# Kernel tuning notes

Measured on AMD Instinct MI355X. Metric: run time of the kernel, lower is better.

Reference implementation:

```python
import jax, jax.numpy as jnp
import numpy as np

EMB = 1024
HEADS = 16
DEPTH = EMB // HEADS
B, S = 8, 1024


def setup_inputs() -> dict:
    key = jax.random.key(0)
    ks = jax.random.split(key, 12)
    sc = 0.02
    return {
        "q": jax.random.normal(ks[0], (B, S, EMB), jnp.float32),
        "k": jax.random.normal(ks[1], (B, S, EMB), jnp.float32),
        "v": jax.random.normal(ks[2], (B, S, EMB), jnp.float32),
        # per-head Dense weights stacked: [H, EMB, DEPTH], biases [H, DEPTH]
        "Wq": jax.random.normal(ks[3], (HEADS, EMB, DEPTH), jnp.float32) * sc,
        "bq": jnp.zeros((HEADS, DEPTH), jnp.float32),
        "Wk": jax.random.normal(ks[4], (HEADS, EMB, DEPTH), jnp.float32) * sc,
        "bk": jnp.zeros((HEADS, DEPTH), jnp.float32),
        "Wv": jax.random.normal(ks[5], (HEADS, EMB, DEPTH), jnp.float32) * sc,
        "bv": jnp.zeros((HEADS, DEPTH), jnp.float32),
        # output Dense: [EMB, EMB], bias [EMB]
        "Wo": jax.random.normal(ks[6], (EMB, EMB), jnp.float32) * sc,
        "bo": jnp.zeros((EMB,), jnp.float32),
    }


def reference(q, k, v, Wq, bq, Wk, bk, Wv, bv, Wo, bo):
    # Per-head Dense projections, batched over heads via einsum.
    # qh: [B, H, S, DEPTH]
    qh = jnp.einsum("bsd,hde->bhse", q, Wq) + bq[None, :, None, :]
    kh = jnp.einsum("bsd,hde->bhse", k, Wk) + bk[None, :, None, :]
    vh = jnp.einsum("bsd,hde->bhse", v, Wv) + bv[None, :, None, :]
    # Scaled dot-product attention per head: logits [B, H, Sq, Sk]
    scale = 1.0 / jnp.sqrt(jnp.asarray(DEPTH, jnp.float32))
    logits = jnp.einsum("bhqe,bhke->bhqk", qh, kh) * scale
    attn = jax.nn.softmax(logits, axis=-1)
    ctx = jnp.einsum("bhqk,bhke->bhqe", attn, vh)  # [B, H, S, DEPTH]
    # concat heads along last axis (head order preserved)
    ctx = jnp.transpose(ctx, (0, 2, 1, 3)).reshape(B, S, EMB)
    return ctx @ Wo + bo
```

## Files before the change

### kernel.cpp

```cpp
#include <hip/hip_runtime.h>
#include <hip/hip_bf16.h>
#include <stdint.h>

typedef __bf16 bf16;
typedef __attribute__((ext_vector_type(8))) __bf16 bf16x8;
typedef __attribute__((ext_vector_type(4))) __bf16 bf16x4;
typedef __attribute__((ext_vector_type(4))) float f32x4;

#define GLD(g, l) __builtin_amdgcn_global_load_lds( \
    (const __attribute__((address_space(1))) void*)(g), \
    (__attribute__((address_space(3))) void*)(l), 16, 0, 0)

__device__ __forceinline__ f32x4 mfma16(bf16x8 a, bf16x8 b, f32x4 c) {
  return __builtin_amdgcn_mfma_f32_16x16x32_bf16(a, b, c, 0, 0, 0);
}
__device__ __forceinline__ float fexp2(float x) {
  return __builtin_amdgcn_exp2f(x);
}

__global__ void wtrans3(const float* __restrict__ Wq, const float* __restrict__ Wk,
                        const float* __restrict__ Wv, bf16* __restrict__ WT)
{
  __shared__ bf16 t[32][33];
  const int w = blockIdx.z;
  const float* W = (w == 0) ? Wq : (w == 1) ? Wk : Wv;
  const int h = blockIdx.x >> 1;
  const int c0 = (blockIdx.x & 1) * 32;
  const int r0 = blockIdx.y * 32;
  const float* s = W + (size_t)h * 65536;
  bf16* d = WT + (size_t)w * (1 << 20) + (size_t)h * 65536;
  const int tx = threadIdx.x, ty = threadIdx.y;
#pragma unroll
  for (int i = 0; i < 32; i += 8)
    t[ty + i][tx] = (bf16)s[(r0 + ty + i) * 64 + c0 + tx];
  __syncthreads();
#pragma unroll
  for (int i = 0; i < 32; i += 8)
    d[(c0 + ty + i) * 1024 + r0 + tx] = t[tx][ty + i];
}

__global__ void wtransO(const float* __restrict__ src, bf16* __restrict__ dst)
{
  __shared__ bf16 t[32][33];
  const int c0 = blockIdx.x * 32, r0 = blockIdx.y * 32;
  const int tx = threadIdx.x, ty = threadIdx.y;
#pragma unroll
  for (int i = 0; i < 32; i += 8)
    t[ty + i][tx] = (bf16)src[(r0 + ty + i) * 1024 + c0 + tx];
  __syncthreads();
#pragma unroll
  for (int i = 0; i < 32; i += 8)
    dst[(c0 + ty + i) * 1024 + r0 + tx] = t[tx][ty + i];
}

__global__ __launch_bounds__(256) void cast2(const float* __restrict__ q,
                                             const float* __restrict__ k,
                                             bf16* __restrict__ qc,
                                             bf16* __restrict__ kc)
{
  const float* s = blockIdx.y ? k : q;
  bf16* d = blockIdx.y ? kc : qc;
  const size_t i = ((size_t)blockIdx.x * 256 + threadIdx.x) * 8;
  float4 a = *(const float4*)(s + i);
  float4 b = *(const float4*)(s + i + 4);
  bf16x8 p;
  p[0] = (bf16)a.x; p[1] = (bf16)a.y; p[2] = (bf16)a.z; p[3] = (bf16)a.w;
  p[4] = (bf16)b.x; p[5] = (bf16)b.y; p[6] = (bf16)b.z; p[7] = (bf16)b.w;
  *(bf16x8*)(d + i) = p;
}

__global__ __launch_bounds__(256) void proj_qkv(
    const bf16* __restrict__ qc, const bf16* __restrict__ kc,
    const float* __restrict__ v, const bf16* __restrict__ WT,
    const float* __restrict__ bq, const float* __restrict__ bk,
    const float* __restrict__ bv, bf16* __restrict__ qh,
    bf16* __restrict__ kh, bf16* __restrict__ vt, float cscale)
{
  __shared__ bf16 S[16384];
  const int tid = threadIdx.x;
  const int wave = tid >> 6, lane = tid & 63;
  const int lr = lane & 15, quad = lane >> 4, kq = quad * 8;
  const int n0 = blockIdx.y * 128;
  const int mseg = blockIdx.x * 128;
  const int seg = mseg >> 13;
  const int m0 = mseg & 8191;
  const int wr = (wave >> 1) * 64, wc = (wave & 1) * 64;

  const float* bias = (seg == 0) ? bq : (seg == 1) ? bk : bv;
  const bf16* Bt = WT + (size_t)seg * (1 << 20);

  f32x4 acc[4][4];
#pragma unroll
  for (int i = 0; i < 4; i++)
#pragma unroll
    for (int j = 0; j < 4; j++)
#pragma unroll
      for (int e = 0; e < 4; e++) acc[i][j][e] = 0.f;

  const int srow = tid >> 2;
  const int sko = (tid & 3) * 8;
  const bf16* bPtr = Bt + (size_t)(n0 + srow) * 1024 + sko;

  if (seg < 2) {
    const bf16* Ab = (seg == 1) ? kc : qc;
    const bf16* aPtr = Ab + (size_t)(m0 + srow) * 1024 + sko;
    GLD(aPtr,             S + tid * 8);
    GLD(aPtr + 64 * 1024, S + 2048 + tid * 8);
    GLD(bPtr,             S + 4096 + tid * 8);
    GLD(bPtr + 64 * 1024, S + 6144 + tid * 8);
    for (int it = 0; it < 32; ++it) {
      const int p = it & 1;
      bf16* buf = S + p * 8192;
      bf16* nbuf = S + (p ^ 1) * 8192;
      __syncthreads();
      if (it + 1 < 32) {
        const int k0 = (it + 1) * 32;
        GLD(aPtr + k0,             nbuf + tid * 8);
        GLD(aPtr + 64 * 1024 + k0, nbuf + 2048 + tid * 8);
        GLD(bPtr + k0,             nbuf + 4096 + tid * 8);
        GLD(bPtr + 64 * 1024 + k0, nbuf + 6144 + tid * 8);
      }
      bf16x8 af[4], bfr[4];
#pragma unroll
      for (int i = 0; i < 4; i++) {
        af[i]  = *(const bf16x8*)(buf + (wr + i * 16 + lr) * 32 + kq);
        bfr[i] = *(const bf16x8*)(buf + 4096 + (wc + i * 16 + lr) * 32 + kq);
      }
#pragma unroll
      for (int im = 0; im < 4; im++)
#pragma unroll
        for (int in = 0; in < 4; in++)
          acc[im][in] = mfma16(af[im], bfr[in], acc[im][in]);
    }
  } else {
    const int ar = tid >> 1, ac2 = (tid & 1) * 16;
    const float* vPtr = v + (size_t)(m0 + ar) * 1024 + ac2;
    float4 f[4];
#pragma unroll
    for (int j = 0; j < 4; j++) f[j] = *(const float4*)(vPtr + j * 4);
    {
      bf16x8 p0, p1;
      p0[0]=(bf16)f[0].x; p0[1]=(bf16)f[0].y; p0[2]=(bf16)f[0].z; p0[3]=(bf16)f[0].w;
      p0[4]=(bf16)f[1].x; p0[5]=(bf16)f[1].y; p0[6]=(bf16)f[1].z; p0[7]=(bf16)f[1].w;
      p1[0]=(bf16)f[2].x; p1[1]=(bf16)f[2].y; p1[2]=(bf16)f[2].z; p1[3]=(bf16)f[2].w;
      p1[4]=(bf16)f[3].x; p1[5]=(bf16)f[3].y; p1[6]=(bf16)f[3].z; p1[7]=(bf16)f[3].w;
      *(bf16x8*)(S + ar * 32 + ac2)     = p0;
      *(bf16x8*)(S + ar * 32 + ac2 + 8) = p1;
    }
    GLD(bPtr,             S + 4096 + tid * 8);
    GLD(bPtr + 64 * 1024, S + 6144 + tid * 8);
    for (int it = 0; it < 32; ++it) {
      const int p = it & 1;
      bf16* buf = S + p * 8192;
      bf16* nbuf = S + (p ^ 1) * 8192;
      __syncthreads();
      const bool more = (it + 1 < 32);
      if (more) {
        const int k0 = (it + 1) * 32;
        GLD(bPtr + k0,             nbuf + 4096 + tid * 8);
        GLD(bPtr + 64 * 1024 + k0, nbuf + 6144 + tid * 8);
#pragma unroll
        for (int j = 0; j < 4; j++) f[j] = *(const float4*)(vPtr + k0 + j * 4);
      }
      bf16x8 af[4], bfr[4];
#pragma unroll
      for (int i = 0; i < 4; i++) {
        af[i]  = *(const bf16x8*)(buf + (wr + i * 16 + lr) * 32 + kq);
        bfr[i] = *(const bf16x8*)(buf + 4096 + (wc + i * 16 + lr) * 32 + kq);
      }
#pragma unroll
      for (int im = 0; im < 4; im++)
#pragma unroll
        for (int in = 0; in < 4; in++)
          acc[im][in] = mfma16(af[im], bfr[in], acc[im][in]);
      if (more) {
        bf16x8 p0, p1;
        p0[0]=(bf16)f[0].x; p0[1]=(bf16)f[0].y; p0[2]=(bf16)f[0].z; p0[3]=(bf16)f[0].w;
        p0[4]=(bf16)f[1].x; p0[5]=(bf16)f[1].y; p0[6]=(bf16)f[1].z; p0[7]=(bf16)f[1].w;
        p1[0]=(bf16)f[2].x; p1[1]=(bf16)f[2].y; p1[2]=(bf16)f[2].z; p1[3]=(bf16)f[2].w;
        p1[4]=(bf16)f[3].x; p1[5]=(bf16)f[3].y; p1[6]=(bf16)f[3].z; p1[7]=(bf16)f[3].w;
        *(bf16x8*)(nbuf + ar * 32 + ac2)     = p0;
        *(bf16x8*)(nbuf + ar * 32 + ac2 + 8) = p1;
      }
    }
  }

  const int qd = quad * 4;
  float bv4[4];
#pragma unroll
  for (int in = 0; in < 4; in++) bv4[in] = bias[n0 + wc + in * 16 + lr];

  if (seg < 2) {
    bf16* C = (seg == 0) ? qh : kh;
    const float cmul = (seg == 0) ? cscale : 1.0f;
#pragma unroll
    for (int im = 0; im < 4; im++) {
      const int row = m0 + wr + im * 16 + qd;
#pragma unroll
      for (int in = 0; in < 4; in++) {
        const int col = n0 + wc + in * 16 + lr;
#pragma unroll
        for (int i = 0; i < 4; i++)
          C[(size_t)(row + i) * 1024 + col] = (bf16)((acc[im][in][i] + bv4[in]) * cmul);
      }
    }
  } else {
#pragma unroll
    for (int im = 0; im < 4; im++) {
      const int row = m0 + wr + im * 16 + qd;
      const int b = row >> 10, sin = row & 1023;
#pragma unroll
      for (int in = 0; in < 4; in++) {
        const int col = n0 + wc + in * 16 + lr;
        const int h = col >> 6, e = col & 63;
        bf16x4 pk;
#pragma unroll
        for (int i = 0; i < 4; i++) pk[i] = (bf16)(acc[im][in][i] + bv4[in]);
        *(bf16x4*)(vt + (size_t)(b * 16 + h) * 65536 + e * 1024 + sin) = pk;
      }
    }
  }
}

__global__ __launch_bounds__(256) void gemm_a16_c32(
    const bf16* __restrict__ A, const bf16* __restrict__ Bt,
    const float* __restrict__ bias, float* __restrict__ C)
{
  __shared__ bf16 S[16384];
  const int tid = threadIdx.x;
  const int wave = tid >> 6, lane = tid & 63;
  const int lr = lane & 15, kq = ((lane >> 4)) * 8;
  const int m0 = blockIdx.x * 128, n0 = blockIdx.y * 128;
  const int wr = (wave >> 1) * 64, wc = (wave & 1) * 64;

  f32x4 acc[4][4];
#pragma unroll
  for (int i = 0; i < 4; i++)
#pragma unroll
    for (int j = 0; j < 4; j++)
#pragma unroll
      for (int e = 0; e < 4; e++) acc[i][j][e] = 0.f;

  const int srow = tid >> 2;
  const int sko = (tid & 3) * 8;
  const bf16* aPtr = A + (size_t)(m0 + srow) * 1024 + sko;
  const bf16* bPtr = Bt + (size_t)(n0 + srow) * 1024 + sko;

  GLD(aPtr,             S + tid * 8);
  GLD(aPtr + 64 * 1024, S + 2048 + tid * 8);
  GLD(bPtr,             S + 4096 + tid * 8);
  GLD(bPtr + 64 * 1024, S + 6144 + tid * 8);
  for (int it = 0; it < 32; ++it) {
    const int p = it & 1;
    bf16* buf = S + p * 8192;
    bf16* nbuf = S + (p ^ 1) * 8192;
    __syncthreads();
    if (it + 1 < 32) {
      const int k0 = (it + 1) * 32;
      GLD(aPtr + k0,             nbuf + tid * 8);
      GLD(aPtr + 64 * 1024 + k0, nbuf + 2048 + tid * 8);
      GLD(bPtr + k0,             nbuf + 4096 + tid * 8);
      GLD(bPtr + 64 * 1024 + k0, nbuf + 6144 + tid * 8);
    }
    bf16x8 af[4], bfr[4];
#pragma unroll
    for (int i = 0; i < 4; i++) {
      af[i]  = *(const bf16x8*)(buf + (wr + i * 16 + lr) * 32 + kq);
      bfr[i] = *(const bf16x8*)(buf + 4096 + (wc + i * 16 + lr) * 32 + kq);
    }
#pragma unroll
    for (int im = 0; im < 4; im++)
#pragma unroll
      for (int in = 0; in < 4; in++)
        acc[im][in] = mfma16(af[im], bfr[in], acc[im][in]);
  }

  const int qd = ((tid & 63) >> 4) * 4;
  float bv4[4];
#pragma unroll
  for (int in = 0; in < 4; in++) bv4[in] = bias[n0 + wc + in * 16 + lr];
#pragma unroll
  for (int im = 0; im < 4; im++) {
    const int row = m0 + wr + im * 16 + qd;
#pragma unroll
    for (int in = 0; in < 4; in++) {
      const int col = n0 + wc + in * 16 + lr;
#pragma unroll
      for (int i = 0; i < 4; i++)
        C[(size_t)(row + i) * 1024 + col] = acc[im][in][i] + bv4[in];
    }
  }
}

__global__ __launch_bounds__(256) void attn_k(
    const bf16* Q, const bf16* __restrict__ Kh,
    const bf16* __restrict__ Vt, bf16* O)
{
  __shared__ bf16 sK[64 * 72];
  __shared__ bf16 sV[64 * 72];
  __shared__ bf16 sP[128 * 72];
  const int h = blockIdx.x, b = blockIdx.y, q0 = blockIdx.z * 128;
  const int tid = threadIdx.x, wave = tid >> 6, lane = tid & 63;
  const int lr = lane & 15, quad = lane >> 4, kq = quad * 8;
  const int wq = wave * 32;

  const bf16* Qb = Q + (size_t)(b * 1024 + q0) * 1024 + h * 64;
  const bf16* Kb = Kh + (size_t)(b * 1024) * 1024 + h * 64;
  const bf16* Vb = Vt + (size_t)(b * 16 + h) * 65536;

  bf16x8 qf[2][2];
#pragma unroll
  for (int rg = 0; rg < 2; rg++)
#pragma unroll
    for (int ks = 0; ks < 2; ks++)
      qf[rg][ks] = *(const bf16x8*)(Qb + (wq + rg * 16 + lr) * 1024 + ks * 32 + kq);

  f32x4 o[2][4];
  float rsum[2][4];
#pragma unroll
  for (int rg = 0; rg < 2; rg++) {
#pragma unroll
    for (int et = 0; et < 4; et++)
#pragma unroll
      for (int e = 0; e < 4; e++) o[rg][et][e] = 0.f;
#pragma unroll
    for (int i = 0; i < 4; i++) rsum[rg][i] = 0.f;
  }

  const int r = tid >> 3;
  const int c = (tid & 7) * 8;

  bf16x8 k1 = *(const bf16x8*)(Kb + (size_t)r * 1024 + c);
  bf16x8 k2 = *(const bf16x8*)(Kb + (size_t)(32 + r) * 1024 + c);
  bf16x8 v1 = *(const bf16x8*)(Vb + (size_t)r * 1024 + c);
  bf16x8 v2 = *(const bf16x8*)(Vb + (size_t)(32 + r) * 1024 + c);

  for (int kv0 = 0; kv0 < 1024; kv0 += 64) {
    __syncthreads();
    *(bf16x8*)(sK + r * 72 + c) = k1;
    *(bf16x8*)(sK + (32 + r) * 72 + c) = k2;
    *(bf16x8*)(sV + r * 72 + c) = v1;
    *(bf16x8*)(sV + (32 + r) * 72 + c) = v2;
    __syncthreads();
    if (kv0 + 64 < 1024) {
      k1 = *(const bf16x8*)(Kb + (size_t)(kv0 + 64 + r) * 1024 + c);
      k2 = *(const bf16x8*)(Kb + (size_t)(kv0 + 96 + r) * 1024 + c);
      v1 = *(const bf16x8*)(Vb + (size_t)r * 1024 + kv0 + 64 + c);
      v2 = *(const bf16x8*)(Vb + (size_t)(32 + r) * 1024 + kv0 + 64 + c);
    }

    f32x4 sc[2][4];
#pragma unroll
    for (int nt = 0; nt < 4; nt++) {
      bf16x8 kf0 = *(const bf16x8*)(sK + (nt * 16 + lr) * 72 + kq);
      bf16x8 kf1 = *(const bf16x8*)(sK + (nt * 16 + lr) * 72 + 32 + kq);
#pragma unroll
      for (int rg = 0; rg < 2; rg++) {
        f32x4 z;
#pragma unroll
        for (int e = 0; e < 4; e++) z[e] = 0.f;
        z = mfma16(qf[rg][0], kf0, z);
        z = mfma16(qf[rg][1], kf1, z);
        sc[rg][nt] = z;
      }
    }

#pragma unroll
    for (int rg = 0; rg < 2; rg++)
#pragma unroll
      for (int i = 0; i < 4; i++) {
        float p0 = fexp2(sc[rg][0][i]);
        float p1 = fexp2(sc[rg][1][i]);
        float p2 = fexp2(sc[rg][2][i]);
        float p3 = fexp2(sc[rg][3][i]);
        rsum[rg][i] += (p0 + p1) + (p2 + p3);
        const int prow = (wq + rg * 16 + quad * 4 + i) * 72;
        sP[prow + 0 * 16 + lr] = (bf16)p0;
        sP[prow + 1 * 16 + lr] = (bf16)p1;
        sP[prow + 2 * 16 + lr] = (bf16)p2;
        sP[prow + 3 * 16 + lr] = (bf16)p3;
      }
    __syncthreads();

#pragma unroll
    for (int et = 0; et < 4; et++) {
      bf16x8 vf0 = *(const bf16x8*)(sV + (et * 16 + lr) * 72 + kq);
      bf16x8 vf1 = *(const bf16x8*)(sV + (et * 16 + lr) * 72 + 32 + kq);
#pragma unroll
      for (int rg = 0; rg < 2; rg++) {
        bf16x8 pa = *(const bf16x8*)(sP + (wq + rg * 16 + lr) * 72 + kq);
        bf16x8 pb = *(const bf16x8*)(sP + (wq + rg * 16 + lr) * 72 + 32 + kq);
        o[rg][et] = mfma16(pa, vf0, o[rg][et]);
        o[rg][et] = mfma16(pb, vf1, o[rg][et]);
      }
    }
  }

#pragma unroll
  for (int rg = 0; rg < 2; rg++)
#pragma unroll
    for (int i = 0; i < 4; i++) {
      float rs = rsum[rg][i];
#pragma unroll
      for (int off = 1; off < 16; off <<= 1)
        rs += __shfl_xor(rs, off, 64);
      rsum[rg][i] = 1.f / rs;
    }

  bf16* Ob = O + (size_t)(b * 1024 + q0) * 1024 + h * 64;
#pragma unroll
  for (int rg = 0; rg < 2; rg++)
#pragma unroll
    for (int i = 0; i < 4; i++) {
      const int row = wq + rg * 16 + quad * 4 + i;
#pragma unroll
      for (int et = 0; et < 4; et++)
        Ob[row * 1024 + et * 16 + lr] = (bf16)(o[rg][et][i] * rsum[rg][i]);
    }
}

extern "C" void kernel_launch(void* const* d_in, const int* in_sizes, int n_in,
                              void* d_out, int out_size, void* d_ws, size_t ws_size,
                              hipStream_t stream)
{
  const float* q  = (const float*)d_in[0];
  const float* k  = (const float*)d_in[1];
  const float* v  = (const float*)d_in[2];
  const float* Wq = (const float*)d_in[3];
  const float* bq = (const float*)d_in[4];
  const float* Wk = (const float*)d_in[5];
  const float* bk = (const float*)d_in[6];
  const float* Wv = (const float*)d_in[7];
  const float* bv = (const float*)d_in[8];
  const float* Wo = (const float*)d_in[9];
  const float* bo = (const float*)d_in[10];
  float* out = (float*)d_out;
  bf16* ws = (bf16*)d_ws;

  const int MB = 1 << 20;
  bf16* WT  = ws;
  bf16* qh  = ws + 3 * MB;
  bf16* kh  = ws + 11 * MB;
  bf16* vt  = ws + 19 * MB;
  bf16* WoT = ws + 27 * MB;
  bf16* qc  = (bf16*)d_out;
  bf16* kc  = (bf16*)d_out + 8 * MB;

  const float cscale = 0.1803368801111601f;

  dim3 tb(32, 8);
  wtrans3<<<dim3(32, 32, 3), tb, 0, stream>>>(Wq, Wk, Wv, WT);
  wtransO<<<dim3(32, 32), tb, 0, stream>>>(Wo, WoT);
  cast2<<<dim3(4096, 2), 256, 0, stream>>>(q, k, qc, kc);

  proj_qkv<<<dim3(192, 8), 256, 0, stream>>>(qc, kc, v, WT, bq, bk, bv,
                                             qh, kh, vt, cscale);

  attn_k<<<dim3(16, 8, 8), 256, 0, stream>>>(qh, kh, vt, qh);

  gemm_a16_c32<<<dim3(64, 8), 256, 0, stream>>>(qh, WoT, bo, out);
}
```

Baseline: 341.6 us.

## Fuse q/k cast into projection and load weight fragments directly into registers

Removes the separate cast2 kernel. All three Q/K/V projection segments now read fp32 activations directly and convert them to bf16 while staging into a padded LDS buffer, using a two-ahead register prefetch. Both GEMM kernels now read B-operand (weight) fragments straight from global memory into registers with a one-step prefetch instead of staging them through LDS. This halves LDS traffic and use and removes a kernel launch plus the bf16 round trip for q and k. The cost is more per-wave global loads of weights, which are redundant across waves, and more register pressure.

```diff
diff --git a/kernel.cpp b/kernel.cpp
--- a/kernel.cpp
+++ b/kernel.cpp
@@ -53,30 +53,14 @@
     dst[(c0 + ty + i) * 1024 + r0 + tx] = t[tx][ty + i];
 }
 
-__global__ __launch_bounds__(256) void cast2(const float* __restrict__ q,
-                                             const float* __restrict__ k,
-                                             bf16* __restrict__ qc,
-                                             bf16* __restrict__ kc)
-{
-  const float* s = blockIdx.y ? k : q;
-  bf16* d = blockIdx.y ? kc : qc;
-  const size_t i = ((size_t)blockIdx.x * 256 + threadIdx.x) * 8;
-  float4 a = *(const float4*)(s + i);
-  float4 b = *(const float4*)(s + i + 4);
-  bf16x8 p;
-  p[0] = (bf16)a.x; p[1] = (bf16)a.y; p[2] = (bf16)a.z; p[3] = (bf16)a.w;
-  p[4] = (bf16)b.x; p[5] = (bf16)b.y; p[6] = (bf16)b.z; p[7] = (bf16)b.w;
-  *(bf16x8*)(d + i) = p;
-}
-
 __global__ __launch_bounds__(256) void proj_qkv(
-    const bf16* __restrict__ qc, const bf16* __restrict__ kc,
-    const float* __restrict__ v, const bf16* __restrict__ WT,
+    const float* __restrict__ Aq, const float* __restrict__ Ak,
+    const float* __restrict__ Av, const bf16* __restrict__ WT,
     const float* __restrict__ bq, const float* __restrict__ bk,
     const float* __restrict__ bv, bf16* __restrict__ qh,
     bf16* __restrict__ kh, bf16* __restrict__ vt, float cscale)
 {
-  __shared__ bf16 S[16384];
+  __shared__ bf16 sA[2][128 * 36];
   const int tid = threadIdx.x;
   const int wave = tid >> 6, lane = tid & 63;
   const int lr = lane & 15, quad = lane >> 4, kq = quad * 8;
@@ -86,6 +70,7 @@
   const int m0 = mseg & 8191;
   const int wr = (wave >> 1) * 64, wc = (wave & 1) * 64;
 
+  const float* A = (seg == 0) ? Aq : (seg == 1) ? Ak : Av;
   const float* bias = (seg == 0) ? bq : (seg == 1) ? bk : bv;
   const bf16* Bt = WT + (size_t)seg * (1 << 20);
 
@@ -97,91 +82,62 @@
 #pragma unroll
       for (int e = 0; e < 4; e++) acc[i][j][e] = 0.f;
 
-  const int srow = tid >> 2;
-  const int sko = (tid & 3) * 8;
-  const bf16* bPtr = Bt + (size_t)(n0 + srow) * 1024 + sko;
-
-  if (seg < 2) {
-    const bf16* Ab = (seg == 1) ? kc : qc;
-    const bf16* aPtr = Ab + (size_t)(m0 + srow) * 1024 + sko;
-    GLD(aPtr,             S + tid * 8);
-    GLD(aPtr + 64 * 1024, S + 2048 + tid * 8);
-    GLD(bPtr,             S + 4096 + tid * 8);
-    GLD(bPtr + 64 * 1024, S + 6144 + tid * 8);
-    for (int it = 0; it < 32; ++it) {
-      const int p = it & 1;
-      bf16* buf = S + p * 8192;
-      bf16* nbuf = S + (p ^ 1) * 8192;
-      __syncthreads();
-      if (it + 1 < 32) {
-        const int k0 = (it + 1) * 32;
-        GLD(aPtr + k0,             nbuf + tid * 8);
-        GLD(aPtr + 64 * 1024 + k0, nbuf + 2048 + tid * 8);
-        GLD(bPtr + k0,             nbuf + 4096 + tid * 8);
-        GLD(bPtr + 64 * 1024 + k0, nbuf + 6144 + tid * 8);
-      }
-      bf16x8 af[4], bfr[4];
-#pragma unroll
-      for (int i = 0; i < 4; i++) {
-        af[i]  = *(const bf16x8*)(buf + (wr + i * 16 + lr) * 32 + kq);
-        bfr[i] = *(const bf16x8*)(buf + 4096 + (wc + i * 16 + lr) * 32 + kq);
-      }
-#pragma unroll
-      for (int im = 0; im < 4; im++)
-#pragma unroll
-        for (int in = 0; in < 4; in++)
-          acc[im][in] = mfma16(af[im], bfr[in], acc[im][in]);
-    }
-  } else {
-    const int ar = tid >> 1, ac2 = (tid & 1) * 16;
-    const float* vPtr = v + (size_t)(m0 + ar) * 1024 + ac2;
-    float4 f[4];
-#pragma unroll
-    for (int j = 0; j < 4; j++) f[j] = *(const float4*)(vPtr + j * 4);
-    {
+  const int ar = tid >> 1, ac = (tid & 1) * 16;
+  const float* aPtr = A + (size_t)(m0 + ar) * 1024 + ac;
+  const bf16* bRow = Bt + (size_t)(n0 + wc + lr) * 1024 + kq;
+
+  float4 f[4];
+#pragma unroll
+  for (int j = 0; j < 4; j++) f[j] = *(const float4*)(aPtr + j * 4);
+  {
+    bf16x8 p0, p1;
+    p0[0]=(bf16)f[0].x; p0[1]=(bf16)f[0].y; p0[2]=(bf16)f[0].z; p0[3]=(bf16)f[0].w;
+    p0[4]=(bf16)f[1].x; p0[5]=(bf16)f[1].y; p0[6]=(bf16)f[1].z; p0[7]=(bf16)f[1].w;
+    p1[0]=(bf16)f[2].x; p1[1]=(bf16)f[2].y; p1[2]=(bf16)f[2].z; p1[3]=(bf16)f[2].w;
+    p1[4]=(bf16)f[3].x; p1[5]=(bf16)f[3].y; p1[6]=(bf16)f[3].z; p1[7]=(bf16)f[3].w;
+    *(bf16x8*)(&sA[0][ar * 36 + ac])     = p0;
+    *(bf16x8*)(&sA[0][ar * 36 + ac + 8]) = p1;
+  }
+  bf16x8 bfr[4], bnx[4];
+#pragma unroll
+  for (int i = 0; i < 4; i++) bfr[i] = *(const bf16x8*)(bRow + i * 16384);
+#pragma unroll
+  for (int j = 0; j < 4; j++) f[j] = *(const float4*)(aPtr + 32 + j * 4);
+
+  for (int it = 0; it < 32; ++it) {
+    const int p = it & 1;
+    __syncthreads();
+    const bool more = (it + 1 < 32);
+    if (more) {
+      const int kn = (it + 1) * 32;
+#pragma unroll
+      for (int i = 0; i < 4; i++)
+        bnx[i] = *(const bf16x8*)(bRow + i * 16384 + kn);
+    }
+    bf16x8 af[4];
+#pragma unroll
+    for (int i = 0; i < 4; i++)
+      af[i] = *(const bf16x8*)(&sA[p][(wr + i * 16 + lr) * 36 + kq]);
+#pragma unroll
+    for (int im = 0; im < 4; im++)
+#pragma unroll
+      for (int in = 0; in < 4; in++)
+        acc[im][in] = mfma16(af[im], bfr[in], acc[im][in]);
+    if (more) {
       bf16x8 p0, p1;
       p0[0]=(bf16)f[0].x; p0[1]=(bf16)f[0].y; p0[2]=(bf16)f[0].z; p0[3]=(bf16)f[0].w;
       p0[4]=(bf16)f[1].x; p0[5]=(bf16)f[1].y; p0[6]=(bf16)f[1].z; p0[7]=(bf16)f[1].w;
       p1[0]=(bf16)f[2].x; p1[1]=(bf16)f[2].y; p1[2]=(bf16)f[2].z; p1[3]=(bf16)f[2].w;
       p1[4]=(bf16)f[3].x; p1[5]=(bf16)f[3].y; p1[6]=(bf16)f[3].z; p1[7]=(bf16)f[3].w;
-      *(bf16x8*)(S + ar * 32 + ac2)     = p0;
-      *(bf16x8*)(S + ar * 32 + ac2 + 8) = p1;
-    }
-    GLD(bPtr,             S + 4096 + tid * 8);
-    GLD(bPtr + 64 * 1024, S + 6144 + tid * 8);
-    for (int it = 0; it < 32; ++it) {
-      const int p = it & 1;
-      bf16* buf = S + p * 8192;
-      bf16* nbuf = S + (p ^ 1) * 8192;
-      __syncthreads();
-      const bool more = (it + 1 < 32);
-      if (more) {
-        const int k0 = (it + 1) * 32;
-        GLD(bPtr + k0,             nbuf + 4096 + tid * 8);
-        GLD(bPtr + 64 * 1024 + k0, nbuf + 6144 + tid * 8);
-#pragma unroll
-        for (int j = 0; j < 4; j++) f[j] = *(const float4*)(vPtr + k0 + j * 4);
-      }
-      bf16x8 af[4], bfr[4];
-#pragma unroll
-      for (int i = 0; i < 4; i++) {
-        af[i]  = *(const bf16x8*)(buf + (wr + i * 16 + lr) * 32 + kq);
-        bfr[i] = *(const bf16x8*)(buf + 4096 + (wc + i * 16 + lr) * 32 + kq);
-      }
-#pragma unroll
-      for (int im = 0; im < 4; im++)
-#pragma unroll
-        for (int in = 0; in < 4; in++)
-          acc[im][in] = mfma16(af[im], bfr[in], acc[im][in]);
-      if (more) {
-        bf16x8 p0, p1;
-        p0[0]=(bf16)f[0].x; p0[1]=(bf16)f[0].y; p0[2]=(bf16)f[0].z; p0[3]=(bf16)f[0].w;
-        p0[4]=(bf16)f[1].x; p0[5]=(bf16)f[1].y; p0[6]=(bf16)f[1].z; p0[7]=(bf16)f[1].w;
-        p1[0]=(bf16)f[2].x; p1[1]=(bf16)f[2].y; p1[2]=(bf16)f[2].z; p1[3]=(bf16)f[2].w;
-        p1[4]=(bf16)f[3].x; p1[5]=(bf16)f[3].y; p1[6]=(bf16)f[3].z; p1[7]=(bf16)f[3].w;
-        *(bf16x8*)(nbuf + ar * 32 + ac2)     = p0;
-        *(bf16x8*)(nbuf + ar * 32 + ac2 + 8) = p1;
-      }
+      *(bf16x8*)(&sA[p ^ 1][ar * 36 + ac])     = p0;
+      *(bf16x8*)(&sA[p ^ 1][ar * 36 + ac + 8]) = p1;
+      if (it + 2 < 32) {
+        const int ka = (it + 2) * 32;
+#pragma unroll
+        for (int j = 0; j < 4; j++) f[j] = *(const float4*)(aPtr + ka + j * 4);
+      }
+#pragma unroll
+      for (int i = 0; i < 4; i++) bfr[i] = bnx[i];
     }
   }
 
@@ -226,10 +182,10 @@
     const bf16* __restrict__ A, const bf16* __restrict__ Bt,
     const float* __restrict__ bias, float* __restrict__ C)
 {
-  __shared__ bf16 S[16384];
+  __shared__ bf16 S[2][4096];
   const int tid = threadIdx.x;
   const int wave = tid >> 6, lane = tid & 63;
-  const int lr = lane & 15, kq = ((lane >> 4)) * 8;
+  const int lr = lane & 15, quad = lane >> 4, kq = quad * 8;
   const int m0 = blockIdx.x * 128, n0 = blockIdx.y * 128;
   const int wr = (wave >> 1) * 64, wc = (wave & 1) * 64;
 
@@ -244,38 +200,42 @@
   const int srow = tid >> 2;
   const int sko = (tid & 3) * 8;
   const bf16* aPtr = A + (size_t)(m0 + srow) * 1024 + sko;
-  const bf16* bPtr = Bt + (size_t)(n0 + srow) * 1024 + sko;
-
-  GLD(aPtr,             S + tid * 8);
-  GLD(aPtr + 64 * 1024, S + 2048 + tid * 8);
-  GLD(bPtr,             S + 4096 + tid * 8);
-  GLD(bPtr + 64 * 1024, S + 6144 + tid * 8);
+  const bf16* bRow = Bt + (size_t)(n0 + wc + lr) * 1024 + kq;
+
+  GLD(aPtr,             &S[0][tid * 8]);
+  GLD(aPtr + 64 * 1024, &S[0][2048 + tid * 8]);
+  bf16x8 bfr[4], bnx[4];
+#pragma unroll
+  for (int i = 0; i < 4; i++) bfr[i] = *(const bf16x8*)(bRow + i * 16384);
+
   for (int it = 0; it < 32; ++it) {
     const int p = it & 1;
-    bf16* buf = S + p * 8192;
-    bf16* nbuf = S + (p ^ 1) * 8192;
     __syncthreads();
-    if (it + 1 < 32) {
-      const int k0 = (it + 1) * 32;
-      GLD(aPtr + k0,             nbuf + tid * 8);
-      GLD(aPtr + 64 * 1024 + k0, nbuf + 2048 + tid * 8);
-      GLD(bPtr + k0,             nbuf + 4096 + tid * 8);
-      GLD(bPtr + 64 * 1024 + k0, nbuf + 6144 + tid * 8);
-    }
-    bf16x8 af[4], bfr[4];
-#pragma unroll
-    for (int i = 0; i < 4; i++) {
-      af[i]  = *(const bf16x8*)(buf + (wr + i * 16 + lr) * 32 + kq);
-      bfr[i] = *(const bf16x8*)(buf + 4096 + (wc + i * 16 + lr) * 32 + kq);
-    }
+    const bool more = (it + 1 < 32);
+    if (more) {
+      const int kn = (it + 1) * 32;
+      GLD(aPtr + kn,             &S[p ^ 1][tid * 8]);
+      GLD(aPtr + 64 * 1024 + kn, &S[p ^ 1][2048 + tid * 8]);
+#pragma unroll
+      for (int i = 0; i < 4; i++)
+        bnx[i] = *(const bf16x8*)(bRow + i * 16384 + kn);
+    }
+    bf16x8 af[4];
+#pragma unroll
+    for (int i = 0; i < 4; i++)
+      af[i] = *(const bf16x8*)(&S[p][(wr + i * 16 + lr) * 32 + kq]);
 #pragma unroll
     for (int im = 0; im < 4; im++)
 #pragma unroll
       for (int in = 0; in < 4; in++)
         acc[im][in] = mfma16(af[im], bfr[in], acc[im][in]);
-  }
-
-  const int qd = ((tid & 63) >> 4) * 4;
+    if (more) {
+#pragma unroll
+      for (int i = 0; i < 4; i++) bfr[i] = bnx[i];
+    }
+  }
+
+  const int qd = quad * 4;
   float bv4[4];
 #pragma unroll
   for (int in = 0; in < 4; in++) bv4[in] = bias[n0 + wc + in * 16 + lr];
@@ -443,17 +403,14 @@
   bf16* kh  = ws + 11 * MB;
   bf16* vt  = ws + 19 * MB;
   bf16* WoT = ws + 27 * MB;
-  bf16* qc  = (bf16*)d_out;
-  bf16* kc  = (bf16*)d_out + 8 * MB;
 
   const float cscale = 0.1803368801111601f;
 
   dim3 tb(32, 8);
   wtrans3<<<dim3(32, 32, 3), tb, 0, stream>>>(Wq, Wk, Wv, WT);
   wtransO<<<dim3(32, 32), tb, 0, stream>>>(Wo, WoT);
-  cast2<<<dim3(4096, 2), 256, 0, stream>>>(q, k, qc, kc);
-
-  proj_qkv<<<dim3(192, 8), 256, 0, stream>>>(qc, kc, v, WT, bq, bk, bv,
+
+  proj_qkv<<<dim3(192, 8), 256, 0, stream>>>(q, k, v, WT, bq, bk, bv,
                                              qh, kh, vt, cscale);
 
   attn_k<<<dim3(16, 8, 8), 256, 0, stream>>>(qh, kh, vt, qh);
```

After: 395.4 us. +15.7%, slower.
